# Kernel optimization log

Hardware: AMD Instinct MI355X
Metric: run time of the kernel (lower is better)

The kernel has to match this reference:

```python
import jax, jax.numpy as jnp
import numpy as np


def setup_inputs() -> dict:
    key = jax.random.key(0)
    ks = jax.random.split(key, 5)
    B, T, in_dim, out_dim = 8, 1024, 4096, 4096
    b_in, b_out, bs_in, bs_out, rank = 16, 16, 256, 256, 128
    std = np.sqrt(0.02).astype(np.float32)
    x = jax.random.normal(ks[0], (B, T, in_dim), dtype=jnp.float32)
    S = jax.random.uniform(ks[1], (b_out, b_in, rank), dtype=jnp.float32)
    U = std * jax.random.normal(ks[2], (b_out, rank, bs_out), dtype=jnp.float32)
    Vt = std * jax.random.normal(ks[3], (b_in, bs_in, rank), dtype=jnp.float32)
    bias = jax.random.normal(ks[4], (out_dim,), dtype=jnp.float32)
    return {"x": x, "S": S, "U": U, "Vt": Vt, "bias": bias}


def _blast_weight(S, U, Vt, in_dim):
    # Faithful to AbstractBlast.weight(eye(in_dim)): pass identity through the
    # block low-rank chain to materialize the dense weight W (in_dim, out_dim).
    b_in, bs_in, rank = Vt.shape
    I = jnp.eye(in_dim, dtype=Vt.dtype)
    # xp: (b_in, in_dim, bs_in) -- block-column slices of the identity
    xp = I.reshape(in_dim, b_in, bs_in).transpose(1, 0, 2)
    y = jnp.einsum('jms,jsr->jmr', xp, Vt)     # (b_in, in_dim, rank)
    z = jnp.einsum('jmr,ojr->omr', y, S)        # (b_out, in_dim, rank)
    out = jnp.einsum('omr,orp->omp', z, U)      # (b_out, in_dim, bs_out)
    W = out.transpose(1, 0, 2).reshape(in_dim, -1)  # (in_dim, out_dim)
    return W


def reference(x, S, U, Vt, bias):
    in_dim = x.shape[-1]
    X = x.reshape(-1, in_dim)                   # to2D
    W = _blast_weight(S, U, Vt, in_dim)
    out = bias + X @ W                          # addmm
    return out.reshape(*x.shape[:-1], -1)       # undo_to2D
```

## Files before the change

### kernel.cpp

```cpp
#include <hip/hip_runtime.h>
#include <hip/hip_bf16.h>


typedef __bf16 bf16x8 __attribute__((ext_vector_type(8)));
typedef __bf16 bf16x4 __attribute__((ext_vector_type(4)));
typedef float  f32x4  __attribute__((ext_vector_type(4)));

#define IN_DIM  4096
#define OUT_DIM 4096
#define NROWS   8192
#define BJ      16
#define BO      16
#define RANK    128

__device__ __forceinline__ bf16x4 cvt4(f32x4 v) {
  bf16x4 r;
  r[0] = (__bf16)v[0]; r[1] = (__bf16)v[1]; r[2] = (__bf16)v[2]; r[3] = (__bf16)v[3];
  return r;
}
__device__ __forceinline__ f32x4 lo4(bf16x8 v) {
  return (f32x4){(float)v[0], (float)v[1], (float)v[2], (float)v[3]};
}
__device__ __forceinline__ f32x4 hi4(bf16x8 v) {
  return (f32x4){(float)v[4], (float)v[5], (float)v[6], (float)v[7]};
}

__global__ __launch_bounds__(256) void prep_frag(
    const float* __restrict__ Vt, const float* __restrict__ U,
    __bf16* __restrict__ vtf, __bf16* __restrict__ utf)
{
  const int NV = BJ * 256 * RANK;
  int v = blockIdx.x * 256 + threadIdx.x;
  if (v < NV) {
    const int e = v & 7, lane = (v >> 3) & 63, ks = (v >> 9) & 7,
              rf = (v >> 12) & 7, j = v >> 15;
    const int l = lane & 15, lh = lane >> 4;
    const int s = ks * 32 + lh * 8 + e, r = rf * 16 + l;
    vtf[v] = (__bf16)Vt[((size_t)(j * 256 + s)) * RANK + r];
  } else {
    const int u = v - NV;
    const int e = u & 7, lane = (u >> 3) & 63, ks = (u >> 9) & 3,
              pf = (u >> 11) & 15, o = u >> 15;
    const int l = lane & 15, lh = lane >> 4;
    const int r = ks * 32 + lh * 8 + e, p = pf * 16 + l;
    utf[u] = (__bf16)U[((size_t)(o * RANK + r)) * 256 + p];
  }
}

__global__ __launch_bounds__(256, 4) void k1_T(
    const float* __restrict__ x, const __bf16* __restrict__ vtf,
    __bf16* __restrict__ T)
{
  __shared__ __bf16 X_lds[64 * 256];

  const int tid  = threadIdx.x;
  const int lane = tid & 63;
  const int w    = tid >> 6;
  const int l15  = lane & 15;
  const int lhi  = lane >> 4;
  const int b    = blockIdx.x;
  const int j    = (b >> 3) & 15;
  const int mt   = (b & 7) * 16 + (b >> 7);
  const size_t rowbase = (size_t)mt * 64;

  #pragma unroll
  for (int i = 0; i < 16; ++i) {
    const int row = w * 16 + i;
    const f32x4 v = __builtin_nontemporal_load(
        (const f32x4*)(x + (rowbase + row) * IN_DIM + j * 256 + lane * 4));
    const int c = (lane >> 1) ^ (row & 15);
    *(bf16x4*)&X_lds[row * 256 + c * 8 + (lane & 1) * 4] = cvt4(v);
  }
  __syncthreads();

  f32x4 acc[2][4];
  #pragma unroll
  for (int a = 0; a < 2; ++a)
    #pragma unroll
    for (int c = 0; c < 4; ++c) acc[a][c] = (f32x4){0.f, 0.f, 0.f, 0.f};

  const __bf16* va = vtf + ((size_t)(j * 8 + w * 2) * 8) * 512 + lane * 8;
  #pragma unroll
  for (int ks = 0; ks < 8; ++ks) {
    bf16x8 bfr[4];
    #pragma unroll
    for (int nf = 0; nf < 4; ++nf) {
      const int c = (ks * 4 + lhi) ^ l15;
      bfr[nf] = *(const bf16x8*)&X_lds[(nf * 16 + l15) * 256 + c * 8];
    }
    const bf16x8 a0 = *(const bf16x8*)(va + (size_t)ks * 512);
    const bf16x8 a1 = *(const bf16x8*)(va + (size_t)(8 + ks) * 512);
    #pragma unroll
    for (int nf = 0; nf < 4; ++nf) {
      acc[0][nf] = __builtin_amdgcn_mfma_f32_16x16x32_bf16(a0, bfr[nf], acc[0][nf], 0, 0, 0);
      acc[1][nf] = __builtin_amdgcn_mfma_f32_16x16x32_bf16(a1, bfr[nf], acc[1][nf], 0, 0, 0);
    }
  }
  #pragma unroll
  for (int rfi = 0; rfi < 2; ++rfi)
    #pragma unroll
    for (int nf = 0; nf < 4; ++nf) {
      *(bf16x4*)&T[((size_t)j * NROWS + rowbase + nf * 16 + l15) * RANK
                   + (w * 2 + rfi) * 16 + lhi * 4] = cvt4(acc[rfi][nf]);
    }
}

__global__ __launch_bounds__(256, 4) void k2_fused(
    const __bf16* __restrict__ T, const float* __restrict__ S,
    const __bf16* __restrict__ utf, const float* __restrict__ bias,
    float* __restrict__ out)
{
  __shared__ float  S_lds[BJ * RANK];
  __shared__ __bf16 u_lds[64 * RANK];

  const int tid = threadIdx.x;
  const int b   = blockIdx.x;
  const int o   = (b >> 3) & 15;
  const int mt  = (b & 7) * 16 + (b >> 7);
  const size_t rowbase = (size_t)mt * 64;

  {
    const float* sb = S + (size_t)o * (BJ * RANK);
    #pragma unroll
    for (int h = 0; h < 2; ++h) {
      const int idx = tid + h * 256;
      *(f32x4*)&S_lds[idx * 4] = *(const f32x4*)(sb + idx * 4);
    }
  }
  __syncthreads();

  {
    const int n  = tid >> 2;
    const int rq = tid & 3;
    const __bf16* tg = T + (rowbase + n) * RANK + rq * 8;
    const size_t jstride = (size_t)NROWS * RANK;
    f32x4 uac[8];
    #pragma unroll
    for (int e = 0; e < 8; ++e) uac[e] = (f32x4){0.f, 0.f, 0.f, 0.f};

    #pragma unroll 4
    for (int jb = 0; jb < BJ; ++jb) {
      const __bf16* tj = tg + (size_t)jb * jstride;
      const bf16x8 tv0 = *(const bf16x8*)(tj);
      const bf16x8 tv1 = *(const bf16x8*)(tj + 32);
      const bf16x8 tv2 = *(const bf16x8*)(tj + 64);
      const bf16x8 tv3 = *(const bf16x8*)(tj + 96);
      const float* sj = &S_lds[jb * RANK + rq * 8];
      uac[0] = *(const f32x4*)(sj +  0) * lo4(tv0) + uac[0];
      uac[1] = *(const f32x4*)(sj +  4) * hi4(tv0) + uac[1];
      uac[2] = *(const f32x4*)(sj + 32) * lo4(tv1) + uac[2];
      uac[3] = *(const f32x4*)(sj + 36) * hi4(tv1) + uac[3];
      uac[4] = *(const f32x4*)(sj + 64) * lo4(tv2) + uac[4];
      uac[5] = *(const f32x4*)(sj + 68) * hi4(tv2) + uac[5];
      uac[6] = *(const f32x4*)(sj + 96) * lo4(tv3) + uac[6];
      uac[7] = *(const f32x4*)(sj + 100) * hi4(tv3) + uac[7];
    }
    #pragma unroll
    for (int k = 0; k < 4; ++k) {
      bf16x8 uw;
      const f32x4 a = uac[2 * k], bb = uac[2 * k + 1];
      uw[0] = (__bf16)a[0];  uw[1] = (__bf16)a[1];  uw[2] = (__bf16)a[2];  uw[3] = (__bf16)a[3];
      uw[4] = (__bf16)bb[0]; uw[5] = (__bf16)bb[1]; uw[6] = (__bf16)bb[2]; uw[7] = (__bf16)bb[3];
      const int swz = (k * 4 + rq) ^ (n & 15);
      *(bf16x8*)&u_lds[n * RANK + swz * 8] = uw;
    }
  }
  __syncthreads();

  {
    const int lane = tid & 63;
    const int w    = tid >> 6;
    const int l15  = lane & 15;
    const int lhi  = lane >> 4;

    f32x4 acc[4][4];
    #pragma unroll
    for (int a = 0; a < 4; ++a)
      #pragma unroll
      for (int c = 0; c < 4; ++c) acc[a][c] = (f32x4){0.f, 0.f, 0.f, 0.f};

    #pragma unroll
    for (int ks = 0; ks < 4; ++ks) {
      bf16x8 ubf[4];
      #pragma unroll
      for (int nf = 0; nf < 4; ++nf) {
        const int swz = (ks * 4 + lhi) ^ l15;
        ubf[nf] = *(const bf16x8*)&u_lds[(nf * 16 + l15) * RANK + swz * 8];
      }
      #pragma unroll
      for (int pi = 0; pi < 4; ++pi) {
        const bf16x8 af = *(const bf16x8*)(
            utf + ((size_t)((o * 16 + w * 4 + pi) * 4 + ks)) * 512 + lane * 8);
        #pragma unroll
        for (int nf = 0; nf < 4; ++nf)
          acc[pi][nf] = __builtin_amdgcn_mfma_f32_16x16x32_bf16(af, ubf[nf], acc[pi][nf], 0, 0, 0);
      }
    }

    #pragma unroll
    for (int pi = 0; pi < 4; ++pi) {
      const int colb = o * 256 + (w * 4 + pi) * 16 + lhi * 4;
      const f32x4 bv = *(const f32x4*)(bias + colb);
      #pragma unroll
      for (int nf = 0; nf < 4; ++nf) {
        __builtin_nontemporal_store(acc[pi][nf] + bv,
            (f32x4*)(out + (rowbase + nf * 16 + l15) * OUT_DIM + colb));
      }
    }
  }
}

extern "C" void kernel_launch(void* const* d_in, const int* in_sizes, int n_in,
                              void* d_out, int out_size, void* d_ws, size_t ws_size,
                              hipStream_t stream) {
  const float* x    = (const float*)d_in[0];
  const float* S    = (const float*)d_in[1];
  const float* U    = (const float*)d_in[2];
  const float* Vt   = (const float*)d_in[3];
  const float* bias = (const float*)d_in[4];
  float* out = (float*)d_out;

  __bf16* vtf = (__bf16*)d_ws;
  __bf16* utf = vtf + (size_t)BJ * 8 * 8 * 512;
  __bf16* T   = utf + (size_t)BO * 16 * 4 * 512;

  prep_frag<<<(2 * 524288) / 256, 256, 0, stream>>>(Vt, U, vtf, utf);
  k1_T<<<(NROWS / 64) * BJ, 256, 0, stream>>>(x, vtf, T);
  k2_fused<<<(NROWS / 64) * BO, 256, 0, stream>>>(T, S, utf, bias, out);
}
```

Before: 100.1 us.

## Process two output blocks per k2 workgroup to reuse loaded T rows

Each k2_fused workgroup now computes two output blocks (o0 and o0+1) instead of one. The T tile is read from global memory once and multiplied against both S slices, so the second pass over T is no longer needed. The cost is double the LDS for S and u, more accumulator registers (launch bounds lowered from 4 to 3 blocks per CU), and half as many workgroups.

```diff
diff --git a/kernel.cpp b/kernel.cpp
--- a/kernel.cpp
+++ b/kernel.cpp
@@ -105,24 +105,25 @@
     }
 }
 
-__global__ __launch_bounds__(256, 4) void k2_fused(
+__global__ __launch_bounds__(256, 3) void k2_fused(
     const __bf16* __restrict__ T, const float* __restrict__ S,
     const __bf16* __restrict__ utf, const float* __restrict__ bias,
     float* __restrict__ out)
 {
-  __shared__ float  S_lds[BJ * RANK];
-  __shared__ __bf16 u_lds[64 * RANK];
+  __shared__ float  S_lds[2 * BJ * RANK];
+  __shared__ __bf16 u_lds[2 * 64 * RANK];
 
   const int tid = threadIdx.x;
   const int b   = blockIdx.x;
-  const int o   = (b >> 3) & 15;
-  const int mt  = (b & 7) * 16 + (b >> 7);
+  const int o2  = (b >> 3) & 7;
+  const int mt  = (b & 7) * 16 + (b >> 6);
+  const int o0  = o2 * 2;
   const size_t rowbase = (size_t)mt * 64;
 
   {
-    const float* sb = S + (size_t)o * (BJ * RANK);
-    #pragma unroll
-    for (int h = 0; h < 2; ++h) {
+    const float* sb = S + (size_t)o0 * (BJ * RANK);
+    #pragma unroll
+    for (int h = 0; h < 4; ++h) {
       const int idx = tid + h * 256;
       *(f32x4*)&S_lds[idx * 4] = *(const f32x4*)(sb + idx * 4);
     }
@@ -134,9 +135,12 @@
     const int rq = tid & 3;
     const __bf16* tg = T + (rowbase + n) * RANK + rq * 8;
     const size_t jstride = (size_t)NROWS * RANK;
-    f32x4 uac[8];
-    #pragma unroll
-    for (int e = 0; e < 8; ++e) uac[e] = (f32x4){0.f, 0.f, 0.f, 0.f};
+    f32x4 a0[8], a1[8];
+    #pragma unroll
+    for (int e = 0; e < 8; ++e) {
+      a0[e] = (f32x4){0.f, 0.f, 0.f, 0.f};
+      a1[e] = (f32x4){0.f, 0.f, 0.f, 0.f};
+    }
 
     #pragma unroll 4
     for (int jb = 0; jb < BJ; ++jb) {
@@ -145,24 +149,44 @@
       const bf16x8 tv1 = *(const bf16x8*)(tj + 32);
       const bf16x8 tv2 = *(const bf16x8*)(tj + 64);
       const bf16x8 tv3 = *(const bf16x8*)(tj + 96);
-      const float* sj = &S_lds[jb * RANK + rq * 8];
-      uac[0] = *(const f32x4*)(sj +  0) * lo4(tv0) + uac[0];
-      uac[1] = *(const f32x4*)(sj +  4) * hi4(tv0) + uac[1];
-      uac[2] = *(const f32x4*)(sj + 32) * lo4(tv1) + uac[2];
-      uac[3] = *(const f32x4*)(sj + 36) * hi4(tv1) + uac[3];
-      uac[4] = *(const f32x4*)(sj + 64) * lo4(tv2) + uac[4];
-      uac[5] = *(const f32x4*)(sj + 68) * hi4(tv2) + uac[5];
-      uac[6] = *(const f32x4*)(sj + 96) * lo4(tv3) + uac[6];
-      uac[7] = *(const f32x4*)(sj + 100) * hi4(tv3) + uac[7];
+      const float* sj0 = &S_lds[jb * RANK + rq * 8];
+      const float* sj1 = sj0 + BJ * RANK;
+      f32x4 tf0 = lo4(tv0), tf1 = hi4(tv0), tf2 = lo4(tv1), tf3 = hi4(tv1);
+      f32x4 tf4 = lo4(tv2), tf5 = hi4(tv2), tf6 = lo4(tv3), tf7 = hi4(tv3);
+      a0[0] = *(const f32x4*)(sj0 +  0) * tf0 + a0[0];
+      a0[1] = *(const f32x4*)(sj0 +  4) * tf1 + a0[1];
+      a0[2] = *(const f32x4*)(sj0 + 32) * tf2 + a0[2];
+      a0[3] = *(const f32x4*)(sj0 + 36) * tf3 + a0[3];
+      a0[4] = *(const f32x4*)(sj0 + 64) * tf4 + a0[4];
+      a0[5] = *(const f32x4*)(sj0 + 68) * tf5 + a0[5];
+      a0[6] = *(const f32x4*)(sj0 + 96) * tf6 + a0[6];
+      a0[7] = *(const f32x4*)(sj0 +100) * tf7 + a0[7];
+      a1[0] = *(const f32x4*)(sj1 +  0) * tf0 + a1[0];
+      a1[1] = *(const f32x4*)(sj1 +  4) * tf1 + a1[1];
+      a1[2] = *(const f32x4*)(sj1 + 32) * tf2 + a1[2];
+      a1[3] = *(const f32x4*)(sj1 + 36) * tf3 + a1[3];
+      a1[4] = *(const f32x4*)(sj1 + 64) * tf4 + a1[4];
+      a1[5] = *(const f32x4*)(sj1 + 68) * tf5 + a1[5];
+      a1[6] = *(const f32x4*)(sj1 + 96) * tf6 + a1[6];
+      a1[7] = *(const f32x4*)(sj1 +100) * tf7 + a1[7];
     }
     #pragma unroll
     for (int k = 0; k < 4; ++k) {
-      bf16x8 uw;
-      const f32x4 a = uac[2 * k], bb = uac[2 * k + 1];
-      uw[0] = (__bf16)a[0];  uw[1] = (__bf16)a[1];  uw[2] = (__bf16)a[2];  uw[3] = (__bf16)a[3];
-      uw[4] = (__bf16)bb[0]; uw[5] = (__bf16)bb[1]; uw[6] = (__bf16)bb[2]; uw[7] = (__bf16)bb[3];
       const int swz = (k * 4 + rq) ^ (n & 15);
-      *(bf16x8*)&u_lds[n * RANK + swz * 8] = uw;
+      {
+        bf16x8 uw;
+        const f32x4 ua = a0[2 * k], ub = a0[2 * k + 1];
+        uw[0]=(__bf16)ua[0]; uw[1]=(__bf16)ua[1]; uw[2]=(__bf16)ua[2]; uw[3]=(__bf16)ua[3];
+        uw[4]=(__bf16)ub[0]; uw[5]=(__bf16)ub[1]; uw[6]=(__bf16)ub[2]; uw[7]=(__bf16)ub[3];
+        *(bf16x8*)&u_lds[n * RANK + swz * 8] = uw;
+      }
+      {
+        bf16x8 uw;
+        const f32x4 ua = a1[2 * k], ub = a1[2 * k + 1];
+        uw[0]=(__bf16)ua[0]; uw[1]=(__bf16)ua[1]; uw[2]=(__bf16)ua[2]; uw[3]=(__bf16)ua[3];
+        uw[4]=(__bf16)ub[0]; uw[5]=(__bf16)ub[1]; uw[6]=(__bf16)ub[2]; uw[7]=(__bf16)ub[3];
+        *(bf16x8*)&u_lds[64 * RANK + n * RANK + swz * 8] = uw;
+      }
     }
   }
   __syncthreads();
@@ -173,38 +197,44 @@
     const int l15  = lane & 15;
     const int lhi  = lane >> 4;
 
-    f32x4 acc[4][4];
-    #pragma unroll
-    for (int a = 0; a < 4; ++a)
+    #pragma unroll
+    for (int q = 0; q < 2; ++q) {
+      const int o = o0 + q;
+      const __bf16* ul = &u_lds[q * 64 * RANK];
+
+      f32x4 acc[4][4];
       #pragma unroll
-      for (int c = 0; c < 4; ++c) acc[a][c] = (f32x4){0.f, 0.f, 0.f, 0.f};
-
-    #pragma unroll
-    for (int ks = 0; ks < 4; ++ks) {
-      bf16x8 ubf[4];
+      for (int a = 0; a < 4; ++a)
+        #pragma unroll
+        for (int c = 0; c < 4; ++c) acc[a][c] = (f32x4){0.f, 0.f, 0.f, 0.f};
+
       #pragma unroll
-      for (int nf = 0; nf < 4; ++nf) {
-        const int swz = (ks * 4 + lhi) ^ l15;
-        ubf[nf] = *(const bf16x8*)&u_lds[(nf * 16 + l15) * RANK + swz * 8];
-      }
+      for (int ks = 0; ks < 4; ++ks) {
+        bf16x8 ubf[4];
+        #pragma unroll
+        for (int nf = 0; nf < 4; ++nf) {
+          const int swz = (ks * 4 + lhi) ^ l15;
+          ubf[nf] = *(const bf16x8*)&ul[(nf * 16 + l15) * RANK + swz * 8];
+        }
+        #pragma unroll
+        for (int pi = 0; pi < 4; ++pi) {
+          const bf16x8 af = *(const bf16x8*)(
+              utf + ((size_t)((o * 16 + w * 4 + pi) * 4 + ks)) * 512 + lane * 8);
+          #pragma unroll
+          for (int nf = 0; nf < 4; ++nf)
+            acc[pi][nf] = __builtin_amdgcn_mfma_f32_16x16x32_bf16(af, ubf[nf], acc[pi][nf], 0, 0, 0);
+        }
+      }
+
       #pragma unroll
       for (int pi = 0; pi < 4; ++pi) {
-        const bf16x8 af = *(const bf16x8*)(
-            utf + ((size_t)((o * 16 + w * 4 + pi) * 4 + ks)) * 512 + lane * 8);
-        #pragma unroll
-        for (int nf = 0; nf < 4; ++nf)
-          acc[pi][nf] = __builtin_amdgcn_mfma_f32_16x16x32_bf16(af, ubf[nf], acc[pi][nf], 0, 0, 0);
-      }
-    }
-
-    #pragma unroll
-    for (int pi = 0; pi < 4; ++pi) {
-      const int colb = o * 256 + (w * 4 + pi) * 16 + lhi * 4;
-      const f32x4 bv = *(const f32x4*)(bias + colb);
-      #pragma unroll
-      for (int nf = 0; nf < 4; ++nf) {
-        __builtin_nontemporal_store(acc[pi][nf] + bv,
-            (f32x4*)(out + (rowbase + nf * 16 + l15) * OUT_DIM + colb));
+        const int colb = o * 256 + (w * 4 + pi) * 16 + lhi * 4;
+        const f32x4 bv = *(const f32x4*)(bias + colb);
+        #pragma unroll
+        for (int nf = 0; nf < 4; ++nf) {
+          __builtin_nontemporal_store(acc[pi][nf] + bv,
+              (f32x4*)(out + (rowbase + nf * 16 + l15) * OUT_DIM + colb));
+        }
       }
     }
   }
@@ -226,5 +256,5 @@
 
   prep_frag<<<(2 * 524288) / 256, 256, 0, stream>>>(Vt, U, vtf, utf);
   k1_T<<<(NROWS / 64) * BJ, 256, 0, stream>>>(x, vtf, T);
-  k2_fused<<<(NROWS / 64) * BO, 256, 0, stream>>>(T, S, utf, bias, out);
-}
+  k2_fused<<<(NROWS / 64) * (BO / 2), 256, 0, stream>>>(T, S, utf, bias, out);
+}
```

Result: slower. 105.4 us (+5.3%).

## Restructure k2 so each block loops over all output blocks reusing T in registers

Applied to the files above, without the earlier changes.

k2 now assigns 16 rows per block and loops over all 16 output blocks, loading the T slice once into registers instead of re-reading it for every output block. S is read straight from global memory (no LDS staging), and the intermediate u tile is double-buffered in LDS with one barrier per output block. This removes the 16x redundant T reads but shrinks MFMA tiles to one 16-row fragment, re-reads utf per output block, and uses regular rather than nontemporal output stores. The grid drops from 2048 to 512 blocks and the launch-bounds occupancy hint is lowered to 3.

```diff
diff --git a/kernel.cpp b/kernel.cpp
--- a/kernel.cpp
+++ b/kernel.cpp
@@ -105,106 +105,73 @@
     }
 }
 
-__global__ __launch_bounds__(256, 4) void k2_fused(
+__global__ __launch_bounds__(256, 3) void k2_fused(
     const __bf16* __restrict__ T, const float* __restrict__ S,
     const __bf16* __restrict__ utf, const float* __restrict__ bias,
     float* __restrict__ out)
 {
-  __shared__ float  S_lds[BJ * RANK];
-  __shared__ __bf16 u_lds[64 * RANK];
+  __shared__ __bf16 u_lds[2][16 * RANK];
 
-  const int tid = threadIdx.x;
-  const int b   = blockIdx.x;
-  const int o   = (b >> 3) & 15;
-  const int mt  = (b & 7) * 16 + (b >> 7);
-  const size_t rowbase = (size_t)mt * 64;
+  const int tid  = threadIdx.x;
+  const int lane = tid & 63;
+  const int w    = tid >> 6;
+  const int l15  = lane & 15;
+  const int lhi  = lane >> 4;
+  const size_t rowbase = (size_t)blockIdx.x * 16;
 
+  const int n  = tid & 15;
+  const int rs = tid >> 4;
+
+  bf16x8 tr[BJ];
   {
-    const float* sb = S + (size_t)o * (BJ * RANK);
+    const __bf16* tg = T + (rowbase + n) * RANK + rs * 8;
+    const size_t jstride = (size_t)NROWS * RANK;
     #pragma unroll
-    for (int h = 0; h < 2; ++h) {
-      const int idx = tid + h * 256;
-      *(f32x4*)&S_lds[idx * 4] = *(const f32x4*)(sb + idx * 4);
+    for (int j = 0; j < BJ; ++j) tr[j] = *(const bf16x8*)(tg + (size_t)j * jstride);
+  }
+
+  for (int o = 0; o < BO; ++o) {
+    {
+      f32x4 u0 = {0.f, 0.f, 0.f, 0.f}, u1 = {0.f, 0.f, 0.f, 0.f};
+      const float* sp = S + ((size_t)o * BJ) * RANK + rs * 8;
+      #pragma unroll 4
+      for (int j = 0; j < BJ; ++j) {
+        const f32x4 s0 = *(const f32x4*)(sp + j * RANK);
+        const f32x4 s1 = *(const f32x4*)(sp + j * RANK + 4);
+        u0 = s0 * lo4(tr[j]) + u0;
+        u1 = s1 * hi4(tr[j]) + u1;
+      }
+      bf16x8 uw;
+      uw[0]=(__bf16)u0[0]; uw[1]=(__bf16)u0[1]; uw[2]=(__bf16)u0[2]; uw[3]=(__bf16)u0[3];
+      uw[4]=(__bf16)u1[0]; uw[5]=(__bf16)u1[1]; uw[6]=(__bf16)u1[2]; uw[7]=(__bf16)u1[3];
+      *(bf16x8*)&u_lds[o & 1][n * RANK + (rs ^ n) * 8] = uw;
     }
-  }
-  __syncthreads();
-
-  {
-    const int n  = tid >> 2;
-    const int rq = tid & 3;
-    const __bf16* tg = T + (rowbase + n) * RANK + rq * 8;
-    const size_t jstride = (size_t)NROWS * RANK;
-    f32x4 uac[8];
-    #pragma unroll
-    for (int e = 0; e < 8; ++e) uac[e] = (f32x4){0.f, 0.f, 0.f, 0.f};
-
-    #pragma unroll 4
-    for (int jb = 0; jb < BJ; ++jb) {
-      const __bf16* tj = tg + (size_t)jb * jstride;
-      const bf16x8 tv0 = *(const bf16x8*)(tj);
-      const bf16x8 tv1 = *(const bf16x8*)(tj + 32);
-      const bf16x8 tv2 = *(const bf16x8*)(tj + 64);
-      const bf16x8 tv3 = *(const bf16x8*)(tj + 96);
-      const float* sj = &S_lds[jb * RANK + rq * 8];
-      uac[0] = *(const f32x4*)(sj +  0) * lo4(tv0) + uac[0];
-      uac[1] = *(const f32x4*)(sj +  4) * hi4(tv0) + uac[1];
-      uac[2] = *(const f32x4*)(sj + 32) * lo4(tv1) + uac[2];
-      uac[3] = *(const f32x4*)(sj + 36) * hi4(tv1) + uac[3];
-      uac[4] = *(const f32x4*)(sj + 64) * lo4(tv2) + uac[4];
-      uac[5] = *(const f32x4*)(sj + 68) * hi4(tv2) + uac[5];
-      uac[6] = *(const f32x4*)(sj + 96) * lo4(tv3) + uac[6];
-      uac[7] = *(const f32x4*)(sj + 100) * hi4(tv3) + uac[7];
-    }
-    #pragma unroll
-    for (int k = 0; k < 4; ++k) {
-      bf16x8 uw;
-      const f32x4 a = uac[2 * k], bb = uac[2 * k + 1];
-      uw[0] = (__bf16)a[0];  uw[1] = (__bf16)a[1];  uw[2] = (__bf16)a[2];  uw[3] = (__bf16)a[3];
-      uw[4] = (__bf16)bb[0]; uw[5] = (__bf16)bb[1]; uw[6] = (__bf16)bb[2]; uw[7] = (__bf16)bb[3];
-      const int swz = (k * 4 + rq) ^ (n & 15);
-      *(bf16x8*)&u_lds[n * RANK + swz * 8] = uw;
-    }
-  }
-  __syncthreads();
-
-  {
-    const int lane = tid & 63;
-    const int w    = tid >> 6;
-    const int l15  = lane & 15;
-    const int lhi  = lane >> 4;
-
-    f32x4 acc[4][4];
-    #pragma unroll
-    for (int a = 0; a < 4; ++a)
-      #pragma unroll
-      for (int c = 0; c < 4; ++c) acc[a][c] = (f32x4){0.f, 0.f, 0.f, 0.f};
-
-    #pragma unroll
-    for (int ks = 0; ks < 4; ++ks) {
+    __syncthreads();
+    {
       bf16x8 ubf[4];
       #pragma unroll
-      for (int nf = 0; nf < 4; ++nf) {
+      for (int ks = 0; ks < 4; ++ks) {
         const int swz = (ks * 4 + lhi) ^ l15;
-        ubf[nf] = *(const bf16x8*)&u_lds[(nf * 16 + l15) * RANK + swz * 8];
+        ubf[ks] = *(const bf16x8*)&u_lds[o & 1][l15 * RANK + swz * 8];
       }
+      f32x4 acc[4];
+      #pragma unroll
+      for (int pi = 0; pi < 4; ++pi) acc[pi] = (f32x4){0.f, 0.f, 0.f, 0.f};
       #pragma unroll
       for (int pi = 0; pi < 4; ++pi) {
-        const bf16x8 af = *(const bf16x8*)(
-            utf + ((size_t)((o * 16 + w * 4 + pi) * 4 + ks)) * 512 + lane * 8);
         #pragma unroll
-        for (int nf = 0; nf < 4; ++nf)
-          acc[pi][nf] = __builtin_amdgcn_mfma_f32_16x16x32_bf16(af, ubf[nf], acc[pi][nf], 0, 0, 0);
+        for (int ks = 0; ks < 4; ++ks) {
+          const bf16x8 af = *(const bf16x8*)(
+              utf + ((size_t)((o * 16 + w * 4 + pi) * 4 + ks)) * 512 + lane * 8);
+          acc[pi] = __builtin_amdgcn_mfma_f32_16x16x32_bf16(af, ubf[ks], acc[pi], 0, 0, 0);
+        }
       }
-    }
-
-    #pragma unroll
-    for (int pi = 0; pi < 4; ++pi) {
-      const int colb = o * 256 + (w * 4 + pi) * 16 + lhi * 4;
-      const f32x4 bv = *(const f32x4*)(bias + colb);
+      float* orow = out + (rowbase + l15) * OUT_DIM + o * 256;
       #pragma unroll
-      for (int nf = 0; nf < 4; ++nf) {
-        __builtin_nontemporal_store(acc[pi][nf] + bv,
-            (f32x4*)(out + (rowbase + nf * 16 + l15) * OUT_DIM + colb));
+      for (int pi = 0; pi < 4; ++pi) {
+        const int cb = (w * 4 + pi) * 16 + lhi * 4;
+        const f32x4 bv = *(const f32x4*)(bias + o * 256 + cb);
+        *(f32x4*)(orow + cb) = acc[pi] + bv;
       }
     }
   }
@@ -226,5 +193,5 @@
 
   prep_frag<<<(2 * 524288) / 256, 256, 0, stream>>>(Vt, U, vtf, utf);
   k1_T<<<(NROWS / 64) * BJ, 256, 0, stream>>>(x, vtf, T);
-  k2_fused<<<(NROWS / 64) * BO, 256, 0, stream>>>(T, S, utf, bias, out);
+  k2_fused<<<NROWS / 16, 256, 0, stream>>>(T, S, utf, bias, out);
 }
```

Result: slower. 181.0 us (+80.8%).
